# Performance work log

Measured on AMD Instinct MI355X. Metric: run time of the kernel, lower is better.

Reference implementation:

```python
import jax, jax.numpy as jnp
import numpy as np

N_NODES = 50000
N_EDGES = 1600000
N_REL = 8
D_IN = 128
D_HID = 128
D_OUT = 64
N_POOL = 256


def setup_inputs() -> dict:
    key = jax.random.key(0)
    ks = jax.random.split(key, 10)
    x = jax.random.uniform(ks[0], (N_NODES, D_IN), dtype=jnp.float32)
    edge_index = jax.random.randint(ks[1], (2, N_EDGES), 0, N_NODES)
    edge_type = jax.random.randint(ks[2], (N_EDGES,), 0, N_REL)
    pool_indices = jax.random.randint(ks[3], (N_POOL,), 0, N_NODES)
    s1 = 1.0 / np.sqrt(D_IN)
    s2 = 1.0 / np.sqrt(D_HID)
    W1 = jax.random.normal(ks[4], (N_REL, D_IN, D_HID), dtype=jnp.float32) * s1
    root1 = jax.random.normal(ks[5], (D_IN, D_HID), dtype=jnp.float32) * s1
    b1 = jnp.zeros((D_HID,), jnp.float32)
    W2 = jax.random.normal(ks[6], (N_REL, D_HID, D_OUT), dtype=jnp.float32) * s2
    root2 = jax.random.normal(ks[7], (D_HID, D_OUT), dtype=jnp.float32) * s2
    b2 = jnp.zeros((D_OUT,), jnp.float32)
    return {"x": x, "edge_index": edge_index, "edge_type": edge_type,
            "pool_indices": pool_indices, "W1": W1, "root1": root1, "b1": b1,
            "W2": W2, "root2": root2, "b2": b2}


def rgcn_layer(h, edge_index, edge_type, W, root, b):
    # PyG RGCNConv: out = h @ root + sum_r mean_{j in N_r(i)} (h_j @ W_r) + b
    src, dst = edge_index[0], edge_index[1]
    n = h.shape[0]
    r = W.shape[0]
    hW = jnp.einsum('nd,rdh->rnh', h, W)          # (R, N, H)
    msg = hW[edge_type, src]                      # (E, H) gather per edge
    seg = edge_type * n + dst                     # per-(relation, dst) segment
    agg = jax.ops.segment_sum(msg, seg, num_segments=r * n)
    agg = agg.reshape(r, n, -1)
    cnt = jax.ops.segment_sum(jnp.ones(msg.shape[0], h.dtype), seg,
                              num_segments=r * n).reshape(r, n, 1)
    mean = agg / jnp.maximum(cnt, 1.0)            # per-relation mean
    return mean.sum(0) + h @ root + b


def reference(x, edge_index, edge_type, pool_indices, W1, root1, b1, W2, root2, b2):
    h = jax.nn.relu(rgcn_layer(x, edge_index, edge_type, W1, root1, b1))
    node_embeddings = rgcn_layer(h, edge_index, edge_type, W2, root2, b2)
    selected_embeddings = node_embeddings[pool_indices]       # (P, D_OUT)
    type_features = x[pool_indices, :3]                       # (P, 3)
    weights = jnp.array([4.0, 1.0, 2.0], dtype=x.dtype)
    entity_weights = type_features @ weights                  # (P,)
    sum_of_weights = jnp.sum(entity_weights) + 1e-9
    pooled = jnp.sum(selected_embeddings * entity_weights[:, None], axis=0,
                     keepdims=True) / sum_of_weights          # (1, D_OUT)
    return pooled
```

## Files before the change

kernel.cpp:

```cpp
#include <hip/hip_runtime.h>

#define N_NODES 50000
#define N_EDGES 1600000
#define N_REL   8
#define D_IN    128
#define D_HID   128
#define D_OUT   64
#define N_POOL  256

#define CAP_S   12288
#define NSEG    (N_REL * CAP_S)
#define BUCKET  32
#define BUCKET2 32
#define NCODE   (N_REL * N_POOL)

typedef short v8s __attribute__((ext_vector_type(8)));
typedef float v4f __attribute__((ext_vector_type(4)));

constexpr size_t OFF_FILLC  = 0;
constexpr size_t OFF_FILLC2 = OFF_FILLC + NSEG;
constexpr size_t ZERO_ELEMS = OFF_FILLC2 + NCODE;
constexpr size_t OFF_PBIT   = ZERO_ELEMS;
constexpr size_t OFF_SBIT   = OFF_PBIT + 2048;
constexpr size_t OFF_CTR    = OFF_SBIT + 2048;
constexpr size_t OFF_PID    = OFF_CTR + 8;
constexpr size_t OFF_SID    = OFF_PID + N_NODES;
constexpr size_t OFF_PNODES = OFF_SID + N_NODES;
constexpr size_t OFF_SNODES = OFF_PNODES + N_POOL;
constexpr size_t OFF_SRCSLOT= OFF_SNODES + CAP_S;
constexpr size_t OFF_ESLOT2 = OFF_SRCSLOT + (size_t)NSEG * BUCKET;
constexpr size_t OFF_AGG1B  = OFF_ESLOT2 + (size_t)NCODE * BUCKET2;
constexpr size_t OFF_XALL   = OFF_AGG1B + (size_t)NSEG * 64;
constexpr size_t OFF_WT     = OFF_XALL + (size_t)N_NODES * 64;
constexpr size_t OFF_H      = OFF_WT + (size_t)1152 * 128 / 2;
constexpr size_t OFF_EMB    = OFF_H + (size_t)CAP_S * D_HID;
constexpr size_t TOTAL_ELEMS= OFF_EMB + (size_t)N_POOL * D_OUT;

__device__ __forceinline__ void atomAddF(float* p, float v) { unsafeAtomicAdd(p, v); }

__device__ __forceinline__ unsigned short f2bf(float f) {
  union { float f; unsigned u; } v; v.f = f;
  unsigned r = v.u + 0x7FFFu + ((v.u >> 16) & 1u);
  return (unsigned short)(r >> 16);
}
__device__ __forceinline__ float bfLo(unsigned v) { return __uint_as_float(v << 16); }
__device__ __forceinline__ float bfHi(unsigned v) { return __uint_as_float(v & 0xFFFF0000u); }

__global__ __launch_bounds__(256) void k_init(
    const int* __restrict__ pool, const float* __restrict__ x,
    const float* __restrict__ W1, const float* __restrict__ root1,
    float* __restrict__ ws) {
  unsigned* pBit = (unsigned*)(ws + OFF_PBIT);
  unsigned* sBit = (unsigned*)(ws + OFF_SBIT);
  int*      ctr  = (int*)(ws + OFF_CTR);
  unsigned long long* xall8 = (unsigned long long*)(ws + OFF_XALL);
  unsigned short* Wt = (unsigned short*)(ws + OFF_WT);
  int tid = threadIdx.x, bid = blockIdx.x;
  int gtid = bid * 256 + tid, gthr = gridDim.x * 256;
  int wave = tid >> 6, lane = tid & 63;

  float4 z = {0.f, 0.f, 0.f, 0.f};
  for (int i = gtid; i < (int)(ZERO_ELEMS / 4); i += gthr) ((float4*)ws)[i] = z;

  if (bid == 0) {
    for (int i = tid; i < 2048; i += 256) { pBit[i] = 0u; sBit[i] = 0u; }
    if (tid < 8) ctr[tid] = 0;
    __syncthreads();
    int node = pool[tid];
    unsigned bit = 1u << (node & 31);
    atomicOr(&pBit[node >> 5], bit);
    atomicOr(&sBit[node >> 5], bit);
  }

  int gw = (bid - 1) * 4 + wave;
  if (bid >= 1 && gw < 288) {
    int kt = gw >> 3, nt = gw & 7;
    int k0 = kt * 32 + ((lane >> 4) << 3);
    int n = nt * 16 + (lane & 15);
    v8s frag;
#pragma unroll
    for (int j = 0; j < 8; j++) {
      int kg = k0 + j;
      float v = (kg < 1024) ? W1[(size_t)kg * D_HID + n]
                            : root1[(size_t)(kg - 1024) * D_HID + n];
      frag[j] = (short)f2bf(v);
    }
    ((v8s*)Wt)[gw * 64 + lane] = frag;
  }

  for (int i = gtid; i < N_NODES * 32; i += gthr) {
    float4 v = ((const float4*)x)[i];
    unsigned lo = ((unsigned)f2bf(v.y) << 16) | f2bf(v.x);
    unsigned hi = ((unsigned)f2bf(v.w) << 16) | f2bf(v.z);
    xall8[i] = (unsigned long long)lo | ((unsigned long long)hi << 32);
  }
}

__global__ __launch_bounds__(256) void k_pass1(
    const int* __restrict__ EI, const unsigned* __restrict__ pBit, unsigned* sBit) {
  int idx = blockIdx.x * 256 + threadIdx.x;
  if (idx >= N_EDGES / 4) return;
  int4 d4 = ((const int4*)(EI + N_EDGES))[idx];
  int d[4] = {d4.x, d4.y, d4.z, d4.w};
#pragma unroll
  for (int i = 0; i < 4; i++) {
    int dst = d[i];
    if ((pBit[dst >> 5] >> (dst & 31)) & 1u) {
      int src = EI[idx * 4 + i];
      atomicOr(&sBit[src >> 5], 1u << (src & 31));
    }
  }
}

__global__ __launch_bounds__(256) void k_compactS(
    const unsigned* __restrict__ sBit, const unsigned* __restrict__ pBit,
    int* sId, int* sNodes, int* pId, int* pNodes, int* ctr) {
  __shared__ int wcnt[4];
  __shared__ int sbase;
  int tid = threadIdx.x, wave = tid >> 6, lane = tid & 63;
  int node = blockIdx.x * 256 + tid;
  bool sp = (node < N_NODES) && ((sBit[node >> 5] >> (node & 31)) & 1u);
  unsigned long long m = __ballot(sp);
  if (lane == 0) wcnt[wave] = __popcll(m);
  __syncthreads();
  if (tid == 0) {
    int tot = wcnt[0] + wcnt[1] + wcnt[2] + wcnt[3];
    sbase = tot ? atomicAdd(&ctr[1], tot) : 0;
  }
  __syncthreads();
  if (sp) {
    int off = sbase;
    for (int w2 = 0; w2 < wave; w2++) off += wcnt[w2];
    int id = off + __popcll(m & ((1ull << lane) - 1ull));
    if (id < CAP_S) { sId[node] = id + 1; sNodes[id] = node; }
    else sId[node] = 0;
  }
  bool pp = (node < N_NODES) && ((pBit[node >> 5] >> (node & 31)) & 1u);
  unsigned long long pm = __ballot(pp);
  if (pm) {
    int leader = __ffsll(pm) - 1;
    int base = 0;
    if (lane == leader) base = atomicAdd(&ctr[0], __popcll(pm));
    base = __shfl(base, leader);
    if (pp) {
      int id = base + __popcll(pm & ((1ull << lane) - 1ull));
      pId[node] = id + 1;
      pNodes[id] = node;
    }
  }
}

__global__ __launch_bounds__(256) void k_fill(
    const int* __restrict__ EI, const int* __restrict__ ET,
    const unsigned* __restrict__ sBit, const unsigned* __restrict__ pBit,
    const int* __restrict__ sId, const int* __restrict__ pId,
    int* __restrict__ fillCtr, int* __restrict__ srcSlot,
    int* __restrict__ fillCtr2, int* __restrict__ eslot2) {
  int idx = blockIdx.x * 256 + threadIdx.x;
  if (idx >= N_EDGES / 4) return;
  int4 d4 = ((const int4*)(EI + N_EDGES))[idx];
  int d[4] = {d4.x, d4.y, d4.z, d4.w};
  bool any = false;
#pragma unroll
  for (int i = 0; i < 4; i++)
    any |= ((sBit[d[i] >> 5] >> (d[i] & 31)) & 1u) != 0u;
  if (!any) return;
  int4 t4 = ((const int4*)ET)[idx];
  int4 s4 = ((const int4*)EI)[idx];
  int t[4] = {t4.x, t4.y, t4.z, t4.w};
  int s[4] = {s4.x, s4.y, s4.z, s4.w};
#pragma unroll
  for (int i = 0; i < 4; i++) {
    int dst = d[i];
    if ((sBit[dst >> 5] >> (dst & 31)) & 1u) {
      int sp = sId[dst];
      if (sp > 0) {
        int seg = ((sp - 1) << 3) + t[i];
        int slot = atomicAdd(&fillCtr[seg], 1);
        if (slot < BUCKET) srcSlot[seg * BUCKET + slot] = s[i];
      }
      if ((pBit[dst >> 5] >> (dst & 31)) & 1u) {
        int code = t[i] * N_POOL + (pId[dst] - 1);
        int sl = sId[s[i]] - 1;
        if (sl >= 0) {
          int slot = atomicAdd(&fillCtr2[code], 1);
          if (slot < BUCKET2) eslot2[code * BUCKET2 + slot] = sl;
        }
      }
    }
  }
}

__global__ __launch_bounds__(256) void k_gather(
    const int* __restrict__ fillCtr, const int* __restrict__ srcSlot,
    const unsigned* __restrict__ xall, const int* __restrict__ ctr,
    unsigned* __restrict__ agg1b) {
  int total = ctr[1] << 3;
  int lane = threadIdx.x & 63;
  int wstride = gridDim.x << 2;
  for (int w = (blockIdx.x << 2) + (threadIdx.x >> 6); w < total; w += wstride) {
    int cnt = fillCtr[w];
    if (cnt > BUCKET) cnt = BUCKET;
    const int* slot = srcSlot + w * BUCKET;
    float a0 = 0.f, a1 = 0.f;
    int i = 0;
    for (; i + 4 <= cnt; i += 4) {
      int s0 = slot[i + 0];
      int s1 = slot[i + 1];
      int s2 = slot[i + 2];
      int s3 = slot[i + 3];
      unsigned v0 = xall[(size_t)s0 * 64 + lane];
      unsigned v1 = xall[(size_t)s1 * 64 + lane];
      unsigned v2 = xall[(size_t)s2 * 64 + lane];
      unsigned v3 = xall[(size_t)s3 * 64 + lane];
      a0 += (bfLo(v0) + bfLo(v1)) + (bfLo(v2) + bfLo(v3));
      a1 += (bfHi(v0) + bfHi(v1)) + (bfHi(v2) + bfHi(v3));
    }
    for (; i < cnt; i++) {
      unsigned v = xall[(size_t)slot[i] * 64 + lane];
      a0 += bfLo(v);
      a1 += bfHi(v);
    }
    float inv = 1.0f / fmaxf((float)cnt, 1.0f);
    agg1b[(size_t)w * 64 + lane] = ((unsigned)f2bf(a1 * inv) << 16) | f2bf(a0 * inv);
  }
}

__global__ __launch_bounds__(256) void k_gemm1(
    const unsigned short* __restrict__ agg1b, const unsigned short* __restrict__ xall,
    const unsigned short* __restrict__ Wt, const float* __restrict__ b1,
    const int* __restrict__ sNodes, const int* __restrict__ ctr,
    float* __restrict__ h) {
  int sCount = ctr[1];
  int s0 = blockIdx.x * 16;
  if (s0 >= sCount) return;
  int wave = threadIdx.x >> 6, lane = threadIdx.x & 63;
  int quad = lane >> 4, mn = lane & 15;
  int srow = s0 + mn;
  int g = (srow < sCount) ? sNodes[srow] : 0;
  v4f acc[2];
  acc[0] = (v4f){0.f, 0.f, 0.f, 0.f};
  acc[1] = (v4f){0.f, 0.f, 0.f, 0.f};
  const v8s* WtF = (const v8s*)Wt;
  for (int kt = 0; kt < 36; kt++) {
    const unsigned short* aptr;
    if (kt < 32) {
      int r = kt >> 2;
      int d0 = (kt & 3) * 32 + quad * 8;
      aptr = agg1b + ((size_t)((srow << 3) + r) * 128 + d0);
    } else {
      int d0 = (kt - 32) * 32 + quad * 8;
      aptr = xall + ((size_t)g * 128 + d0);
    }
    v8s afrag = *(const v8s*)aptr;
    const v8s* wrow = WtF + (size_t)(kt * 8 + wave * 2) * 64 + lane;
    acc[0] = __builtin_amdgcn_mfma_f32_16x16x32_bf16(afrag, wrow[0],  acc[0], 0, 0, 0);
    acc[1] = __builtin_amdgcn_mfma_f32_16x16x32_bf16(afrag, wrow[64], acc[1], 0, 0, 0);
  }
#pragma unroll
  for (int nt = 0; nt < 2; nt++) {
    int col = (wave * 2 + nt) * 16 + mn;
    float bias = b1[col];
#pragma unroll
    for (int reg = 0; reg < 4; reg++) {
      int s = s0 + quad * 4 + reg;
      if (s < sCount)
        h[(size_t)s * D_HID + col] = fmaxf(acc[nt][reg] + bias, 0.0f);
    }
  }
}

__global__ __launch_bounds__(256) void k_gemm2(
    const float* __restrict__ W2, const float* __restrict__ root2,
    const float* __restrict__ b2,
    const int* __restrict__ fillCtr2, const int* __restrict__ eslot2,
    const int* __restrict__ pNodes, const int* __restrict__ sId,
    const int* __restrict__ ctr, const float* __restrict__ h,
    float* __restrict__ emb) {
  __shared__ float a[N_REL * D_HID + D_HID];
  __shared__ float partial[256];
  int pl = blockIdx.x;
  if (pl >= ctr[0]) return;
  int tid = threadIdx.x, wave = tid >> 6, lane = tid & 63;
#pragma unroll
  for (int rr = 0; rr < 2; rr++) {
    int r = wave * 2 + rr;
    int code = r * N_POOL + pl;
    int cnt = fillCtr2[code]; if (cnt > BUCKET2) cnt = BUCKET2;
    const int* sl = eslot2 + code * BUCKET2;
    float s0 = 0.f, s1 = 0.f;
    for (int i = 0; i < cnt; i++) {
      float2 v = ((const float2*)h)[(size_t)sl[i] * 64 + lane];
      s0 += v.x; s1 += v.y;
    }
    float inv = 1.0f / fmaxf((float)cnt, 1.0f);
    a[r * 128 + lane * 2]     = s0 * inv;
    a[r * 128 + lane * 2 + 1] = s1 * inv;
  }
  if (tid < 128) {
    int slp = sId[pNodes[pl]] - 1;
    a[1024 + tid] = h[(size_t)slp * D_HID + tid];
  }
  __syncthreads();
  int lo = wave * 288, hi = lo + 288;
  float acc = 0.0f;
  int hiW = (hi < 1024) ? hi : 1024;
#pragma unroll 8
  for (int k = lo; k < hiW; k++) acc += a[k] * W2[(size_t)k * D_OUT + lane];
  int loR = (lo > 1024) ? lo : 1024;
#pragma unroll 8
  for (int k = loR; k < hi; k++) acc += a[k] * root2[(size_t)(k - 1024) * D_OUT + lane];
  partial[tid] = acc;
  __syncthreads();
  if (tid < 64) {
    float r4 = partial[tid] + partial[tid + 64] + partial[tid + 128] + partial[tid + 192];
    emb[(size_t)pl * D_OUT + tid] = r4 + b2[tid];
  }
}

__global__ __launch_bounds__(256) void k_pool(
    const float* __restrict__ x, const int* __restrict__ pool,
    const int* __restrict__ pId, const float* __restrict__ emb,
    float* __restrict__ out) {
  __shared__ float ew[N_POOL];
  __shared__ int pls[N_POOL];
  __shared__ float part[4][64];
  int tid = threadIdx.x, wave = tid >> 6, lane = tid & 63;
  int node = pool[tid];
  const float* xr = x + (size_t)node * D_IN;
  ew[tid] = 4.0f * xr[0] + 1.0f * xr[1] + 2.0f * xr[2];
  pls[tid] = pId[node] - 1;
  __syncthreads();
  float acc = 0.0f;
  int j0 = wave * 64;
#pragma unroll 8
  for (int j = j0; j < j0 + 64; j++)
    acc += ew[j] * emb[(size_t)pls[j] * D_OUT + lane];
  part[wave][lane] = acc;
  __syncthreads();
  if (tid < 64) {
    float sw = 0.0f;
    for (int j = 0; j < N_POOL; j++) sw += ew[j];
    float r4 = part[0][tid] + part[1][tid] + part[2][tid] + part[3][tid];
    out[tid] = r4 / (sw + 1e-9f);
  }
}

extern "C" void kernel_launch(void* const* d_in, const int* in_sizes, int n_in,
                              void* d_out, int out_size, void* d_ws, size_t ws_size,
                              hipStream_t stream) {
  const float* x     = (const float*)d_in[0];
  const int*   EI    = (const int*)  d_in[1];
  const int*   ET    = (const int*)  d_in[2];
  const int*   pool  = (const int*)  d_in[3];
  const float* W1    = (const float*)d_in[4];
  const float* root1 = (const float*)d_in[5];
  const float* b1    = (const float*)d_in[6];
  const float* W2    = (const float*)d_in[7];
  const float* root2 = (const float*)d_in[8];
  const float* b2    = (const float*)d_in[9];
  float* out = (float*)d_out;
  float* ws  = (float*)d_ws;

  int*      fillCtr = (int*)(ws + OFF_FILLC);
  int*      fillCtr2= (int*)(ws + OFF_FILLC2);
  unsigned* pBit    = (unsigned*)(ws + OFF_PBIT);
  unsigned* sBit    = (unsigned*)(ws + OFF_SBIT);
  int*      ctr     = (int*)(ws + OFF_CTR);
  int*      pId     = (int*)(ws + OFF_PID);
  int*      sId     = (int*)(ws + OFF_SID);
  int*      pNodes  = (int*)(ws + OFF_PNODES);
  int*      sNodes  = (int*)(ws + OFF_SNODES);
  int*      srcSlot = (int*)(ws + OFF_SRCSLOT);
  int*      eslot2  = (int*)(ws + OFF_ESLOT2);
  unsigned* agg1b   = (unsigned*)(ws + OFF_AGG1B);
  unsigned* xall    = (unsigned*)(ws + OFF_XALL);
  unsigned short* Wt = (unsigned short*)(ws + OFF_WT);
  float*    h       = ws + OFF_H;
  float*    emb     = ws + OFF_EMB;

  k_init<<<1024, 256, 0, stream>>>(pool, x, W1, root1, ws);
  k_pass1<<<(N_EDGES / 4 + 255) / 256, 256, 0, stream>>>(EI, pBit, sBit);
  k_compactS<<<(N_NODES + 255) / 256, 256, 0, stream>>>(sBit, pBit, sId, sNodes, pId, pNodes, ctr);
  k_fill<<<(N_EDGES / 4 + 255) / 256, 256, 0, stream>>>(
      EI, ET, sBit, pBit, sId, pId, fillCtr, srcSlot, fillCtr2, eslot2);
  k_gather<<<2048, 256, 0, stream>>>(fillCtr, srcSlot, xall, ctr, agg1b);
  k_gemm1<<<CAP_S / 16, 256, 0, stream>>>(
      (const unsigned short*)agg1b, (const unsigned short*)xall, Wt, b1, sNodes, ctr, h);
  k_gemm2<<<N_POOL, 256, 0, stream>>>(
      W2, root2, b2, fillCtr2, eslot2, pNodes, sId, ctr, h, emb);
  k_pool<<<1, 256, 0, stream>>>(x, pool, pId, emb, out);
}
```

Baseline: 188.0 us.

## Fuse neighbor gather into layer-1 MFMA GEMM and fold pooling into layer-2 kernel

The per-segment mean aggregation is now computed inside the layer-1 GEMM kernel and staged in swizzled LDS, so the bf16 aggregate no longer round-trips through global memory. The final pooling step runs in the last block of the layer-2 kernel, detected with an atomic counter and fences, which removes two kernel launches. The costs are that gather parallelism is now tied to GEMM blocks (768 blocks doing serial 16-step gathers), and correctness depends on ctr[2] being zero at launch.

```diff
diff --git a/kernel.cpp b/kernel.cpp
--- a/kernel.cpp
+++ b/kernel.cpp
@@ -29,14 +29,11 @@
 constexpr size_t OFF_SNODES = OFF_PNODES + N_POOL;
 constexpr size_t OFF_SRCSLOT= OFF_SNODES + CAP_S;
 constexpr size_t OFF_ESLOT2 = OFF_SRCSLOT + (size_t)NSEG * BUCKET;
-constexpr size_t OFF_AGG1B  = OFF_ESLOT2 + (size_t)NCODE * BUCKET2;
-constexpr size_t OFF_XALL   = OFF_AGG1B + (size_t)NSEG * 64;
+constexpr size_t OFF_XALL   = OFF_ESLOT2 + (size_t)NCODE * BUCKET2;
 constexpr size_t OFF_WT     = OFF_XALL + (size_t)N_NODES * 64;
 constexpr size_t OFF_H      = OFF_WT + (size_t)1152 * 128 / 2;
 constexpr size_t OFF_EMB    = OFF_H + (size_t)CAP_S * D_HID;
 constexpr size_t TOTAL_ELEMS= OFF_EMB + (size_t)N_POOL * D_OUT;
-
-__device__ __forceinline__ void atomAddF(float* p, float v) { unsafeAtomicAdd(p, v); }
 
 __device__ __forceinline__ unsigned short f2bf(float f) {
   union { float f; unsigned u; } v; v.f = f;
@@ -191,141 +188,151 @@
   }
 }
 
-__global__ __launch_bounds__(256) void k_gather(
+__global__ __launch_bounds__(256) void k_gemmA(
     const int* __restrict__ fillCtr, const int* __restrict__ srcSlot,
-    const unsigned* __restrict__ xall, const int* __restrict__ ctr,
-    unsigned* __restrict__ agg1b) {
-  int total = ctr[1] << 3;
-  int lane = threadIdx.x & 63;
-  int wstride = gridDim.x << 2;
-  for (int w = (blockIdx.x << 2) + (threadIdx.x >> 6); w < total; w += wstride) {
-    int cnt = fillCtr[w];
-    if (cnt > BUCKET) cnt = BUCKET;
-    const int* slot = srcSlot + w * BUCKET;
-    float a0 = 0.f, a1 = 0.f;
-    int i = 0;
-    for (; i + 4 <= cnt; i += 4) {
-      int s0 = slot[i + 0];
-      int s1 = slot[i + 1];
-      int s2 = slot[i + 2];
-      int s3 = slot[i + 3];
-      unsigned v0 = xall[(size_t)s0 * 64 + lane];
-      unsigned v1 = xall[(size_t)s1 * 64 + lane];
-      unsigned v2 = xall[(size_t)s2 * 64 + lane];
-      unsigned v3 = xall[(size_t)s3 * 64 + lane];
-      a0 += (bfLo(v0) + bfLo(v1)) + (bfLo(v2) + bfLo(v3));
-      a1 += (bfHi(v0) + bfHi(v1)) + (bfHi(v2) + bfHi(v3));
-    }
-    for (; i < cnt; i++) {
-      unsigned v = xall[(size_t)slot[i] * 64 + lane];
-      a0 += bfLo(v);
-      a1 += bfHi(v);
-    }
-    float inv = 1.0f / fmaxf((float)cnt, 1.0f);
-    agg1b[(size_t)w * 64 + lane] = ((unsigned)f2bf(a1 * inv) << 16) | f2bf(a0 * inv);
-  }
-}
-
-__global__ __launch_bounds__(256) void k_gemm1(
-    const unsigned short* __restrict__ agg1b, const unsigned short* __restrict__ xall,
-    const unsigned short* __restrict__ Wt, const float* __restrict__ b1,
-    const int* __restrict__ sNodes, const int* __restrict__ ctr,
-    float* __restrict__ h) {
-  int sCount = ctr[1];
+    const unsigned* __restrict__ xall, const unsigned short* __restrict__ Wt,
+    const float* __restrict__ b1, const int* __restrict__ sNodes,
+    const int* __restrict__ ctr, float* __restrict__ h) {
+  __shared__ unsigned lds[128 * 64];
+  int sCount = ctr[1]; if (sCount > CAP_S) sCount = CAP_S;
   int s0 = blockIdx.x * 16;
   if (s0 >= sCount) return;
-  int wave = threadIdx.x >> 6, lane = threadIdx.x & 63;
+  int tid = threadIdx.x, wave = tid >> 6, lane = tid & 63;
+  int segBase = s0 << 3;
+
+  for (int j = 0; j < 16; j++) {
+    int LA = wave * 32 + j, LB = LA + 16;
+    int cA = fillCtr[segBase + LA]; if (cA > BUCKET) cA = BUCKET;
+    int cB = fillCtr[segBase + LB]; if (cB > BUCKET) cB = BUCKET;
+    const int* sA = srcSlot + (size_t)(segBase + LA) * BUCKET;
+    const int* sB = srcSlot + (size_t)(segBase + LB) * BUCKET;
+    float a0A = 0.f, a1A = 0.f, a0B = 0.f, a1B = 0.f;
+    int mx = cA > cB ? cA : cB;
+    for (int i = 0; i < mx; i += 4) {
+#pragma unroll
+      for (int k2 = 0; k2 < 4; k2++) {
+        int ii = i + k2;
+        if (ii < cA) {
+          unsigned v = xall[(size_t)sA[ii] * 64 + lane];
+          a0A += bfLo(v); a1A += bfHi(v);
+        }
+      }
+#pragma unroll
+      for (int k2 = 0; k2 < 4; k2++) {
+        int ii = i + k2;
+        if (ii < cB) {
+          unsigned v = xall[(size_t)sB[ii] * 64 + lane];
+          a0B += bfLo(v); a1B += bfHi(v);
+        }
+      }
+    }
+    float invA = 1.0f / fmaxf((float)cA, 1.0f);
+    float invB = 1.0f / fmaxf((float)cB, 1.0f);
+    unsigned pA = ((unsigned)f2bf(a1A * invA) << 16) | f2bf(a0A * invA);
+    unsigned pB = ((unsigned)f2bf(a1B * invB) << 16) | f2bf(a0B * invB);
+    lds[LA * 64 + ((((lane >> 2) ^ (LA >> 3)) << 2) | (lane & 3))] = pA;
+    lds[LB * 64 + ((((lane >> 2) ^ (LB >> 3)) << 2) | (lane & 3))] = pB;
+  }
+  __syncthreads();
+
   int quad = lane >> 4, mn = lane & 15;
   int srow = s0 + mn;
   int g = (srow < sCount) ? sNodes[srow] : 0;
-  v4f acc[2];
-  acc[0] = (v4f){0.f, 0.f, 0.f, 0.f};
-  acc[1] = (v4f){0.f, 0.f, 0.f, 0.f};
+  v4f acc0 = (v4f){0.f, 0.f, 0.f, 0.f};
+  v4f acc1 = (v4f){0.f, 0.f, 0.f, 0.f};
   const v8s* WtF = (const v8s*)Wt;
+#pragma unroll
   for (int kt = 0; kt < 36; kt++) {
-    const unsigned short* aptr;
+    v8s afrag;
     if (kt < 32) {
-      int r = kt >> 2;
-      int d0 = (kt & 3) * 32 + quad * 8;
-      aptr = agg1b + ((size_t)((srow << 3) + r) * 128 + d0);
+      int row = mn * 8 + (kt >> 2);
+      int c16 = (((kt & 3) << 2) | quad) ^ mn;
+      afrag = *(const v8s*)&lds[row * 64 + (c16 << 2)];
     } else {
       int d0 = (kt - 32) * 32 + quad * 8;
-      aptr = xall + ((size_t)g * 128 + d0);
-    }
-    v8s afrag = *(const v8s*)aptr;
+      afrag = *(const v8s*)((const unsigned short*)xall + (size_t)g * 128 + d0);
+    }
     const v8s* wrow = WtF + (size_t)(kt * 8 + wave * 2) * 64 + lane;
-    acc[0] = __builtin_amdgcn_mfma_f32_16x16x32_bf16(afrag, wrow[0],  acc[0], 0, 0, 0);
-    acc[1] = __builtin_amdgcn_mfma_f32_16x16x32_bf16(afrag, wrow[64], acc[1], 0, 0, 0);
-  }
-#pragma unroll
-  for (int nt = 0; nt < 2; nt++) {
-    int col = (wave * 2 + nt) * 16 + mn;
-    float bias = b1[col];
-#pragma unroll
-    for (int reg = 0; reg < 4; reg++) {
-      int s = s0 + quad * 4 + reg;
-      if (s < sCount)
-        h[(size_t)s * D_HID + col] = fmaxf(acc[nt][reg] + bias, 0.0f);
-    }
-  }
-}
-
-__global__ __launch_bounds__(256) void k_gemm2(
+    acc0 = __builtin_amdgcn_mfma_f32_16x16x32_bf16(afrag, wrow[0],  acc0, 0, 0, 0);
+    acc1 = __builtin_amdgcn_mfma_f32_16x16x32_bf16(afrag, wrow[64], acc1, 0, 0, 0);
+  }
+  int col0 = wave * 32 + mn;
+  int col1 = col0 + 16;
+  float bv0 = b1[col0], bv1 = b1[col1];
+#pragma unroll
+  for (int reg = 0; reg < 4; reg++) {
+    int s = s0 + quad * 4 + reg;
+    if (s < sCount) {
+      h[(size_t)s * D_HID + col0] = fmaxf(acc0[reg] + bv0, 0.0f);
+      h[(size_t)s * D_HID + col1] = fmaxf(acc1[reg] + bv1, 0.0f);
+    }
+  }
+}
+
+__global__ __launch_bounds__(256) void k_gemmB(
+    const float* __restrict__ x, const int* __restrict__ pool,
     const float* __restrict__ W2, const float* __restrict__ root2,
-    const float* __restrict__ b2,
-    const int* __restrict__ fillCtr2, const int* __restrict__ eslot2,
-    const int* __restrict__ pNodes, const int* __restrict__ sId,
-    const int* __restrict__ ctr, const float* __restrict__ h,
-    float* __restrict__ emb) {
-  __shared__ float a[N_REL * D_HID + D_HID];
-  __shared__ float partial[256];
+    const float* __restrict__ b2, const int* __restrict__ fillCtr2,
+    const int* __restrict__ eslot2, const int* __restrict__ pNodes,
+    const int* __restrict__ sId, const int* __restrict__ pId,
+    int* __restrict__ ctr, const float* __restrict__ h,
+    float* __restrict__ emb, float* __restrict__ out) {
+  __shared__ float smem[1408];
+  __shared__ int lastFlag;
   int pl = blockIdx.x;
-  if (pl >= ctr[0]) return;
   int tid = threadIdx.x, wave = tid >> 6, lane = tid & 63;
-#pragma unroll
-  for (int rr = 0; rr < 2; rr++) {
-    int r = wave * 2 + rr;
-    int code = r * N_POOL + pl;
-    int cnt = fillCtr2[code]; if (cnt > BUCKET2) cnt = BUCKET2;
-    const int* sl = eslot2 + code * BUCKET2;
-    float s0 = 0.f, s1 = 0.f;
-    for (int i = 0; i < cnt; i++) {
-      float2 v = ((const float2*)h)[(size_t)sl[i] * 64 + lane];
-      s0 += v.x; s1 += v.y;
-    }
-    float inv = 1.0f / fmaxf((float)cnt, 1.0f);
-    a[r * 128 + lane * 2]     = s0 * inv;
-    a[r * 128 + lane * 2 + 1] = s1 * inv;
-  }
-  if (tid < 128) {
-    int slp = sId[pNodes[pl]] - 1;
-    a[1024 + tid] = h[(size_t)slp * D_HID + tid];
-  }
-  __syncthreads();
-  int lo = wave * 288, hi = lo + 288;
-  float acc = 0.0f;
-  int hiW = (hi < 1024) ? hi : 1024;
+  int pCount = ctr[0];
+  if (pl < pCount) {
+    float* a = smem;
+    float* partial = smem + 1152;
+#pragma unroll
+    for (int rr = 0; rr < 2; rr++) {
+      int r = wave * 2 + rr;
+      int code = r * N_POOL + pl;
+      int cnt = fillCtr2[code]; if (cnt > BUCKET2) cnt = BUCKET2;
+      const int* sl = eslot2 + code * BUCKET2;
+      float s0 = 0.f, s1 = 0.f;
+      for (int i = 0; i < cnt; i++) {
+        float2 v = ((const float2*)h)[(size_t)sl[i] * 64 + lane];
+        s0 += v.x; s1 += v.y;
+      }
+      float inv = 1.0f / fmaxf((float)cnt, 1.0f);
+      a[r * 128 + lane * 2]     = s0 * inv;
+      a[r * 128 + lane * 2 + 1] = s1 * inv;
+    }
+    if (tid < 128) {
+      int slp = sId[pNodes[pl]] - 1;
+      a[1024 + tid] = h[(size_t)slp * D_HID + tid];
+    }
+    __syncthreads();
+    int lo = wave * 288, hi = lo + 288;
+    float acc = 0.0f;
+    int hiW = (hi < 1024) ? hi : 1024;
 #pragma unroll 8
-  for (int k = lo; k < hiW; k++) acc += a[k] * W2[(size_t)k * D_OUT + lane];
-  int loR = (lo > 1024) ? lo : 1024;
+    for (int k = lo; k < hiW; k++) acc += a[k] * W2[(size_t)k * D_OUT + lane];
+    int loR = (lo > 1024) ? lo : 1024;
 #pragma unroll 8
-  for (int k = loR; k < hi; k++) acc += a[k] * root2[(size_t)(k - 1024) * D_OUT + lane];
-  partial[tid] = acc;
-  __syncthreads();
-  if (tid < 64) {
-    float r4 = partial[tid] + partial[tid + 64] + partial[tid + 128] + partial[tid + 192];
-    emb[(size_t)pl * D_OUT + tid] = r4 + b2[tid];
-  }
-}
-
-__global__ __launch_bounds__(256) void k_pool(
-    const float* __restrict__ x, const int* __restrict__ pool,
-    const int* __restrict__ pId, const float* __restrict__ emb,
-    float* __restrict__ out) {
-  __shared__ float ew[N_POOL];
-  __shared__ int pls[N_POOL];
-  __shared__ float part[4][64];
-  int tid = threadIdx.x, wave = tid >> 6, lane = tid & 63;
+    for (int k = loR; k < hi; k++) acc += a[k] * root2[(size_t)(k - 1024) * D_OUT + lane];
+    partial[tid] = acc;
+    __syncthreads();
+    if (tid < 64) {
+      float r4 = partial[tid] + partial[tid + 64] + partial[tid + 128] + partial[tid + 192];
+      emb[(size_t)pl * D_OUT + tid] = r4 + b2[tid];
+    }
+  }
+  __syncthreads();
+  if (tid == 0) {
+    __threadfence();
+    int old = __hip_atomic_fetch_add(&ctr[2], 1, __ATOMIC_ACQ_REL,
+                                     __HIP_MEMORY_SCOPE_AGENT);
+    lastFlag = (old == (int)gridDim.x - 1) ? 1 : 0;
+  }
+  __syncthreads();
+  if (lastFlag == 0) return;
+  __threadfence();
+  float* ew = smem;
+  int*   pls = (int*)(smem + 256);
+  float* part = smem + 512;
   int node = pool[tid];
   const float* xr = x + (size_t)node * D_IN;
   ew[tid] = 4.0f * xr[0] + 1.0f * xr[1] + 2.0f * xr[2];
@@ -336,12 +343,12 @@
 #pragma unroll 8
   for (int j = j0; j < j0 + 64; j++)
     acc += ew[j] * emb[(size_t)pls[j] * D_OUT + lane];
-  part[wave][lane] = acc;
+  part[wave * 64 + lane] = acc;
   __syncthreads();
   if (tid < 64) {
     float sw = 0.0f;
     for (int j = 0; j < N_POOL; j++) sw += ew[j];
-    float r4 = part[0][tid] + part[1][tid] + part[2][tid] + part[3][tid];
+    float r4 = part[tid] + part[64 + tid] + part[128 + tid] + part[192 + tid];
     out[tid] = r4 / (sw + 1e-9f);
   }
 }
@@ -373,7 +380,6 @@
   int*      sNodes  = (int*)(ws + OFF_SNODES);
   int*      srcSlot = (int*)(ws + OFF_SRCSLOT);
   int*      eslot2  = (int*)(ws + OFF_ESLOT2);
-  unsigned* agg1b   = (unsigned*)(ws + OFF_AGG1B);
   unsigned* xall    = (unsigned*)(ws + OFF_XALL);
   unsigned short* Wt = (unsigned short*)(ws + OFF_WT);
   float*    h       = ws + OFF_H;
@@ -384,10 +390,8 @@
   k_compactS<<<(N_NODES + 255) / 256, 256, 0, stream>>>(sBit, pBit, sId, sNodes, pId, pNodes, ctr);
   k_fill<<<(N_EDGES / 4 + 255) / 256, 256, 0, stream>>>(
       EI, ET, sBit, pBit, sId, pId, fillCtr, srcSlot, fillCtr2, eslot2);
-  k_gather<<<2048, 256, 0, stream>>>(fillCtr, srcSlot, xall, ctr, agg1b);
-  k_gemm1<<<CAP_S / 16, 256, 0, stream>>>(
-      (const unsigned short*)agg1b, (const unsigned short*)xall, Wt, b1, sNodes, ctr, h);
-  k_gemm2<<<N_POOL, 256, 0, stream>>>(
-      W2, root2, b2, fillCtr2, eslot2, pNodes, sId, ctr, h, emb);
-  k_pool<<<1, 256, 0, stream>>>(x, pool, pId, emb, out);
-}
+  k_gemmA<<<CAP_S / 16, 256, 0, stream>>>(
+      fillCtr, srcSlot, xall, Wt, b1, sNodes, ctr, h);
+  k_gemmB<<<N_POOL, 256, 0, stream>>>(
+      x, pool, W2, root2, b2, fillCtr2, eslot2, pNodes, sId, pId, ctr, h, emb, out);
+}
```

New measurement: 249.9 us. 1.33x slower.

## Fuse layer-2 GEMM with pooling via last-block reduction and widen gemm1 tiles

Applied to the files above, without the earlier changes.

Merges k_gemm2 and k_pool into a single kernel. Each of 128 blocks handles two pool nodes so the W2/root2 loads are shared. The last block to finish, detected with an atomic counter, then performs the weighted pooling, which removes one kernel launch. Separately, gemm1 now computes 32 rows per block with four MFMA accumulators so each weight fragment is used twice. The atomic counter ctr[2] must be zeroed every call, and the added sCount clamps are safety fixes.

```diff
diff --git a/kernel.cpp b/kernel.cpp
--- a/kernel.cpp
+++ b/kernel.cpp
@@ -36,8 +36,6 @@
 constexpr size_t OFF_EMB    = OFF_H + (size_t)CAP_S * D_HID;
 constexpr size_t TOTAL_ELEMS= OFF_EMB + (size_t)N_POOL * D_OUT;
 
-__device__ __forceinline__ void atomAddF(float* p, float v) { unsafeAtomicAdd(p, v); }
-
 __device__ __forceinline__ unsigned short f2bf(float f) {
   union { float f; unsigned u; } v; v.f = f;
   unsigned r = v.u + 0x7FFFu + ((v.u >> 16) & 1u);
@@ -195,13 +193,14 @@
     const int* __restrict__ fillCtr, const int* __restrict__ srcSlot,
     const unsigned* __restrict__ xall, const int* __restrict__ ctr,
     unsigned* __restrict__ agg1b) {
-  int total = ctr[1] << 3;
+  int sCount = ctr[1]; if (sCount > CAP_S) sCount = CAP_S;
+  int total = sCount << 3;
   int lane = threadIdx.x & 63;
   int wstride = gridDim.x << 2;
   for (int w = (blockIdx.x << 2) + (threadIdx.x >> 6); w < total; w += wstride) {
     int cnt = fillCtr[w];
     if (cnt > BUCKET) cnt = BUCKET;
-    const int* slot = srcSlot + w * BUCKET;
+    const int* slot = srcSlot + (size_t)w * BUCKET;
     float a0 = 0.f, a1 = 0.f;
     int i = 0;
     for (; i + 4 <= cnt; i += 4) {
@@ -231,101 +230,137 @@
     const unsigned short* __restrict__ Wt, const float* __restrict__ b1,
     const int* __restrict__ sNodes, const int* __restrict__ ctr,
     float* __restrict__ h) {
-  int sCount = ctr[1];
-  int s0 = blockIdx.x * 16;
+  int sCount = ctr[1]; if (sCount > CAP_S) sCount = CAP_S;
+  int s0 = blockIdx.x * 32;
   if (s0 >= sCount) return;
   int wave = threadIdx.x >> 6, lane = threadIdx.x & 63;
   int quad = lane >> 4, mn = lane & 15;
-  int srow = s0 + mn;
-  int g = (srow < sCount) ? sNodes[srow] : 0;
-  v4f acc[2];
-  acc[0] = (v4f){0.f, 0.f, 0.f, 0.f};
-  acc[1] = (v4f){0.f, 0.f, 0.f, 0.f};
+  int srow0 = s0 + mn, srow1 = s0 + 16 + mn;
+  int g0 = (srow0 < sCount) ? sNodes[srow0] : 0;
+  int g1 = (srow1 < sCount) ? sNodes[srow1] : 0;
+  v4f acc00 = (v4f){0.f,0.f,0.f,0.f}, acc01 = (v4f){0.f,0.f,0.f,0.f};
+  v4f acc10 = (v4f){0.f,0.f,0.f,0.f}, acc11 = (v4f){0.f,0.f,0.f,0.f};
   const v8s* WtF = (const v8s*)Wt;
   for (int kt = 0; kt < 36; kt++) {
-    const unsigned short* aptr;
+    const unsigned short *ap0, *ap1;
     if (kt < 32) {
       int r = kt >> 2;
       int d0 = (kt & 3) * 32 + quad * 8;
-      aptr = agg1b + ((size_t)((srow << 3) + r) * 128 + d0);
+      ap0 = agg1b + ((size_t)((srow0 << 3) + r) * 128 + d0);
+      ap1 = agg1b + ((size_t)((srow1 << 3) + r) * 128 + d0);
     } else {
       int d0 = (kt - 32) * 32 + quad * 8;
-      aptr = xall + ((size_t)g * 128 + d0);
-    }
-    v8s afrag = *(const v8s*)aptr;
+      ap0 = xall + ((size_t)g0 * 128 + d0);
+      ap1 = xall + ((size_t)g1 * 128 + d0);
+    }
+    v8s af0 = *(const v8s*)ap0;
+    v8s af1 = *(const v8s*)ap1;
     const v8s* wrow = WtF + (size_t)(kt * 8 + wave * 2) * 64 + lane;
-    acc[0] = __builtin_amdgcn_mfma_f32_16x16x32_bf16(afrag, wrow[0],  acc[0], 0, 0, 0);
-    acc[1] = __builtin_amdgcn_mfma_f32_16x16x32_bf16(afrag, wrow[64], acc[1], 0, 0, 0);
-  }
-#pragma unroll
-  for (int nt = 0; nt < 2; nt++) {
-    int col = (wave * 2 + nt) * 16 + mn;
-    float bias = b1[col];
-#pragma unroll
-    for (int reg = 0; reg < 4; reg++) {
-      int s = s0 + quad * 4 + reg;
-      if (s < sCount)
-        h[(size_t)s * D_HID + col] = fmaxf(acc[nt][reg] + bias, 0.0f);
-    }
-  }
-}
-
-__global__ __launch_bounds__(256) void k_gemm2(
+    v8s bf0 = wrow[0], bf1 = wrow[64];
+    acc00 = __builtin_amdgcn_mfma_f32_16x16x32_bf16(af0, bf0, acc00, 0, 0, 0);
+    acc01 = __builtin_amdgcn_mfma_f32_16x16x32_bf16(af0, bf1, acc01, 0, 0, 0);
+    acc10 = __builtin_amdgcn_mfma_f32_16x16x32_bf16(af1, bf0, acc10, 0, 0, 0);
+    acc11 = __builtin_amdgcn_mfma_f32_16x16x32_bf16(af1, bf1, acc11, 0, 0, 0);
+  }
+  int col0 = wave * 32 + mn;
+  int col1 = col0 + 16;
+  float bv0 = b1[col0], bv1 = b1[col1];
+#pragma unroll
+  for (int reg = 0; reg < 4; reg++) {
+    int sA = s0 + quad * 4 + reg;
+    int sB = sA + 16;
+    if (sA < sCount) {
+      h[(size_t)sA * D_HID + col0] = fmaxf(acc00[reg] + bv0, 0.0f);
+      h[(size_t)sA * D_HID + col1] = fmaxf(acc01[reg] + bv1, 0.0f);
+    }
+    if (sB < sCount) {
+      h[(size_t)sB * D_HID + col0] = fmaxf(acc10[reg] + bv0, 0.0f);
+      h[(size_t)sB * D_HID + col1] = fmaxf(acc11[reg] + bv1, 0.0f);
+    }
+  }
+}
+
+__global__ __launch_bounds__(256) void k_gemmB(
+    const float* __restrict__ x, const int* __restrict__ pool,
     const float* __restrict__ W2, const float* __restrict__ root2,
-    const float* __restrict__ b2,
-    const int* __restrict__ fillCtr2, const int* __restrict__ eslot2,
-    const int* __restrict__ pNodes, const int* __restrict__ sId,
-    const int* __restrict__ ctr, const float* __restrict__ h,
-    float* __restrict__ emb) {
-  __shared__ float a[N_REL * D_HID + D_HID];
-  __shared__ float partial[256];
-  int pl = blockIdx.x;
-  if (pl >= ctr[0]) return;
+    const float* __restrict__ b2, const int* __restrict__ fillCtr2,
+    const int* __restrict__ eslot2, const int* __restrict__ pNodes,
+    const int* __restrict__ sId, const int* __restrict__ pId,
+    int* __restrict__ ctr, const float* __restrict__ h,
+    float* __restrict__ emb, float* __restrict__ out) {
+  __shared__ float a0[1152], a1[1152];
+  __shared__ float p0[256], p1[256];
+  __shared__ int lastFlag;
   int tid = threadIdx.x, wave = tid >> 6, lane = tid & 63;
-#pragma unroll
-  for (int rr = 0; rr < 2; rr++) {
-    int r = wave * 2 + rr;
-    int code = r * N_POOL + pl;
-    int cnt = fillCtr2[code]; if (cnt > BUCKET2) cnt = BUCKET2;
-    const int* sl = eslot2 + code * BUCKET2;
-    float s0 = 0.f, s1 = 0.f;
-    for (int i = 0; i < cnt; i++) {
-      float2 v = ((const float2*)h)[(size_t)sl[i] * 64 + lane];
-      s0 += v.x; s1 += v.y;
-    }
-    float inv = 1.0f / fmaxf((float)cnt, 1.0f);
-    a[r * 128 + lane * 2]     = s0 * inv;
-    a[r * 128 + lane * 2 + 1] = s1 * inv;
-  }
-  if (tid < 128) {
-    int slp = sId[pNodes[pl]] - 1;
-    a[1024 + tid] = h[(size_t)slp * D_HID + tid];
-  }
-  __syncthreads();
-  int lo = wave * 288, hi = lo + 288;
-  float acc = 0.0f;
-  int hiW = (hi < 1024) ? hi : 1024;
-#pragma unroll 8
-  for (int k = lo; k < hiW; k++) acc += a[k] * W2[(size_t)k * D_OUT + lane];
-  int loR = (lo > 1024) ? lo : 1024;
-#pragma unroll 8
-  for (int k = loR; k < hi; k++) acc += a[k] * root2[(size_t)(k - 1024) * D_OUT + lane];
-  partial[tid] = acc;
-  __syncthreads();
-  if (tid < 64) {
-    float r4 = partial[tid] + partial[tid + 64] + partial[tid + 128] + partial[tid + 192];
-    emb[(size_t)pl * D_OUT + tid] = r4 + b2[tid];
-  }
-}
-
-__global__ __launch_bounds__(256) void k_pool(
-    const float* __restrict__ x, const int* __restrict__ pool,
-    const int* __restrict__ pId, const float* __restrict__ emb,
-    float* __restrict__ out) {
-  __shared__ float ew[N_POOL];
-  __shared__ int pls[N_POOL];
-  __shared__ float part[4][64];
-  int tid = threadIdx.x, wave = tid >> 6, lane = tid & 63;
+  int pCount = ctr[0];
+  int pl0 = blockIdx.x, pl1 = blockIdx.x + 128;
+  bool do0 = pl0 < pCount, do1 = pl1 < pCount;
+#pragma unroll
+  for (int n2 = 0; n2 < 2; n2++) {
+    int pl = n2 ? pl1 : pl0;
+    float* a = n2 ? a1 : a0;
+    if (pl < pCount) {
+#pragma unroll
+      for (int rr = 0; rr < 2; rr++) {
+        int r = wave * 2 + rr;
+        int code = r * N_POOL + pl;
+        int cnt = fillCtr2[code]; if (cnt > BUCKET2) cnt = BUCKET2;
+        const int* sl = eslot2 + code * BUCKET2;
+        float s0 = 0.f, s1 = 0.f;
+        for (int i = 0; i < cnt; i++) {
+          float2 v = ((const float2*)h)[(size_t)sl[i] * 64 + lane];
+          s0 += v.x; s1 += v.y;
+        }
+        float inv = 1.0f / fmaxf((float)cnt, 1.0f);
+        a[r * 128 + lane * 2]     = s0 * inv;
+        a[r * 128 + lane * 2 + 1] = s1 * inv;
+      }
+      if (tid < 128) {
+        int slp = sId[pNodes[pl]] - 1;
+        a[1024 + tid] = h[(size_t)slp * D_HID + tid];
+      }
+    }
+  }
+  __syncthreads();
+  if (do0 || do1) {
+    int lo = wave * 288, hi = lo + 288;
+    float acc0 = 0.0f, acc1 = 0.0f;
+    int hiW = (hi < 1024) ? hi : 1024;
+#pragma unroll 4
+    for (int k = lo; k < hiW; k++) {
+      float w = W2[(size_t)k * D_OUT + lane];
+      acc0 += a0[k] * w; acc1 += a1[k] * w;
+    }
+    int loR = (lo > 1024) ? lo : 1024;
+#pragma unroll 4
+    for (int k = loR; k < hi; k++) {
+      float w = root2[(size_t)(k - 1024) * D_OUT + lane];
+      acc0 += a0[k] * w; acc1 += a1[k] * w;
+    }
+    p0[tid] = acc0; p1[tid] = acc1;
+    __syncthreads();
+    if (tid < 64) {
+      if (do0)
+        emb[(size_t)pl0 * D_OUT + tid] =
+            p0[tid] + p0[tid + 64] + p0[tid + 128] + p0[tid + 192] + b2[tid];
+      if (do1)
+        emb[(size_t)pl1 * D_OUT + tid] =
+            p1[tid] + p1[tid + 64] + p1[tid + 128] + p1[tid + 192] + b2[tid];
+    }
+  }
+  __syncthreads();
+  if (tid == 0) {
+    __threadfence();
+    int old = __hip_atomic_fetch_add(&ctr[2], 1, __ATOMIC_ACQ_REL,
+                                     __HIP_MEMORY_SCOPE_AGENT);
+    lastFlag = (old == (int)gridDim.x - 1) ? 1 : 0;
+  }
+  __syncthreads();
+  if (lastFlag == 0) return;
+  __threadfence();
+  float* ew = a0;
+  int*   pls = (int*)p0;
+  float* part = p1;
   int node = pool[tid];
   const float* xr = x + (size_t)node * D_IN;
   ew[tid] = 4.0f * xr[0] + 1.0f * xr[1] + 2.0f * xr[2];
@@ -336,12 +371,12 @@
 #pragma unroll 8
   for (int j = j0; j < j0 + 64; j++)
     acc += ew[j] * emb[(size_t)pls[j] * D_OUT + lane];
-  part[wave][lane] = acc;
+  part[wave * 64 + lane] = acc;
   __syncthreads();
   if (tid < 64) {
     float sw = 0.0f;
     for (int j = 0; j < N_POOL; j++) sw += ew[j];
-    float r4 = part[0][tid] + part[1][tid] + part[2][tid] + part[3][tid];
+    float r4 = part[tid] + part[64 + tid] + part[128 + tid] + part[192 + tid];
     out[tid] = r4 / (sw + 1e-9f);
   }
 }
@@ -385,9 +420,8 @@
   k_fill<<<(N_EDGES / 4 + 255) / 256, 256, 0, stream>>>(
       EI, ET, sBit, pBit, sId, pId, fillCtr, srcSlot, fillCtr2, eslot2);
   k_gather<<<2048, 256, 0, stream>>>(fillCtr, srcSlot, xall, ctr, agg1b);
-  k_gemm1<<<CAP_S / 16, 256, 0, stream>>>(
+  k_gemm1<<<CAP_S / 32, 256, 0, stream>>>(
       (const unsigned short*)agg1b, (const unsigned short*)xall, Wt, b1, sNodes, ctr, h);
-  k_gemm2<<<N_POOL, 256, 0, stream>>>(
-      W2, root2, b2, fillCtr2, eslot2, pNodes, sId, ctr, h, emb);
-  k_pool<<<1, 256, 0, stream>>>(x, pool, pId, emb, out);
-}
+  k_gemmB<<<128, 256, 0, stream>>>(
+      x, pool, W2, root2, b2, fillCtr2, eslot2, pNodes, sId, pId, ctr, h, emb, out);
+}
```

Result: slower. 208.6 us (+11.0%).
